# Kernel optimization log

Measured on AMD Instinct MI355X. Metric: run time of the kernel, lower is better.

The kernel has to match this reference:

```python
import jax, jax.numpy as jnp
import numpy as np

T, B, D, H = 512, 64, 512, 512


def setup_inputs() -> dict:
    key = jax.random.key(0)
    k_x, k_wi, k_wh = jax.random.split(key, 3)
    x = jax.random.normal(k_x, (T, B, D), dtype=jnp.float32)
    h0 = jnp.zeros((B, H), dtype=jnp.float32)
    # orthogonal(sqrt(2))-like scale approximated with scaled normal weights
    Wi = jax.random.normal(k_wi, (D, 3 * H), dtype=jnp.float32) * (1.0 / np.sqrt(D))
    Wh = jax.random.normal(k_wh, (H, 3 * H), dtype=jnp.float32) * (1.0 / np.sqrt(H))
    bi = jnp.zeros((3 * H,), dtype=jnp.float32)
    bhn = jnp.zeros((H,), dtype=jnp.float32)
    return {"x": x, "h0": h0, "Wi": Wi, "Wh": Wh, "bi": bi, "bhn": bhn}


def reference(x, h0, Wi, Wh, bi, bhn):
    # Flax GRUCell scanned over time. Gate order: (r, z, n).
    # Input path has bias bi; hidden path is bias-free except candidate (bhn).
    def step(h, xt):
        gi = xt @ Wi + bi              # [B, 3H]
        gh = h @ Wh                    # [B, 3H]
        i_r, i_z, i_n = jnp.split(gi, 3, axis=-1)
        h_r, h_z, h_n = jnp.split(gh, 3, axis=-1)
        r = jax.nn.sigmoid(i_r + h_r)
        z = jax.nn.sigmoid(i_z + h_z)
        n = jnp.tanh(i_n + r * (h_n + bhn))
        h_new = (1.0 - z) * n + z * h  # [B, H]
        return h_new, h_new            # y == new hidden state in GRUCell

    _, ys = jax.lax.scan(step, h0, x)  # ys: [T, B, H]; final carry == ys[-1]
    return ys
```

## Files before the change

kernel.cpp:

```cpp
#include <hip/hip_runtime.h>


#define T_STEPS 512
#define NWORK 32
#define CWG 8
#define NCL 4
#define NB_LAUNCH 256
#define FSTRIDE 16

typedef __attribute__((ext_vector_type(8))) short bhalf8;
typedef __attribute__((ext_vector_type(4))) float floatx4;

__device__ inline float bf2f(unsigned short u) {
  union { unsigned u; float f; } v; v.u = ((unsigned)u) << 16; return v.f;
}
__device__ inline unsigned short f2bf(float f) {
  union { float f; unsigned u; } v; v.f = f;
  unsigned x = v.u;
  return (unsigned short)((x + 0x7fffu + ((x >> 16) & 1u)) >> 16);
}

__device__ inline void gload_lds16(const void* g, void* l) {
  __builtin_amdgcn_global_load_lds(
      (const __attribute__((address_space(1))) void*)g,
      (__attribute__((address_space(3))) void*)l, 16, 0, 0);
}

#define O_BAR 0
#define O_HB  4096
#define O_WIT 69632
#define O_WHT 1642496
#define O_GI  3215360
#define O_XB  103878656ULL
#define WS_NEED 137433088ULL

__device__ inline unsigned short* HS(char* ws, int t) {
  return (t == 0) ? (unsigned short*)(ws + O_HB)
                  : (unsigned short*)(ws + O_XB + (long)(t - 1) * 65536);
}

__global__ void prep_kernel(const float* __restrict__ x, const float* __restrict__ h0,
                            const float* __restrict__ Wi, const float* __restrict__ Wh,
                            char* __restrict__ ws) {
  unsigned short* Xb  = (unsigned short*)(ws + O_XB);
  unsigned short* WiT = (unsigned short*)(ws + O_WIT);
  unsigned short* WhT = (unsigned short*)(ws + O_WHT);
  unsigned short* Hb0 = (unsigned short*)(ws + O_HB);
  int* bar = (int*)(ws + O_BAR);
  const long NX = 16777216, NW = 786432, NH = 32768;
  const long total = NX + 2 * NW + NH + 1024;
  for (long i = (long)blockIdx.x * blockDim.x + threadIdx.x; i < total;
       i += (long)gridDim.x * blockDim.x) {
    if (i < NX) {
      Xb[i] = f2bf(x[i]);
    } else if (i < NX + NW) {
      long j = i - NX;
      long n = j >> 9, k = j & 511;
      WiT[j] = f2bf(Wi[k * 1536 + n]);
    } else if (i < NX + 2 * NW) {
      long j = i - NX - NW;
      long n = j >> 9, k = j & 511;
      WhT[j] = f2bf(Wh[k * 1536 + n]);
    } else if (i < NX + 2 * NW + NH) {
      long j = i - NX - 2 * NW;
      Hb0[j] = f2bf(h0[j]);
    } else {
      bar[i - (NX + 2 * NW + NH)] = 0;
    }
  }
}

__global__ void gi_gemm(const unsigned short* __restrict__ Xb,
                        const unsigned short* __restrict__ WiT,
                        const float* __restrict__ bi,
                        unsigned short* __restrict__ Gi) {
  __shared__ unsigned short As[128 * 32];
  __shared__ unsigned short Bs[128 * 32];
  const int tid  = threadIdx.x;
  const int m0   = blockIdx.x * 128;
  const int n0   = blockIdx.y * 128;
  const int lane = tid & 63, wv = tid >> 6;
  const int quad = lane >> 4, l16 = lane & 15;
  const int wm = (wv & 1) * 64, wn = (wv >> 1) * 64;
  const int sr = tid >> 1, sc = (tid & 1) * 16;

  floatx4 acc[4][4] = {};

  for (int kb = 0; kb < 16; ++kb) {
    const int k0 = kb * 32;
    __syncthreads();
    *(bhalf8*)(&As[sr * 32 + sc])     = *(const bhalf8*)(&Xb[(long)(m0 + sr) * 512 + k0 + sc]);
    *(bhalf8*)(&As[sr * 32 + sc + 8]) = *(const bhalf8*)(&Xb[(long)(m0 + sr) * 512 + k0 + sc + 8]);
    *(bhalf8*)(&Bs[sr * 32 + sc])     = *(const bhalf8*)(&WiT[(long)(n0 + sr) * 512 + k0 + sc]);
    *(bhalf8*)(&Bs[sr * 32 + sc + 8]) = *(const bhalf8*)(&WiT[(long)(n0 + sr) * 512 + k0 + sc + 8]);
    __syncthreads();

    bhalf8 af[4], bf[4];
#pragma unroll
    for (int i = 0; i < 4; ++i)
      af[i] = *(const bhalf8*)(&As[(wm + i * 16 + l16) * 32 + quad * 8]);
#pragma unroll
    for (int j = 0; j < 4; ++j)
      bf[j] = *(const bhalf8*)(&Bs[(wn + j * 16 + l16) * 32 + quad * 8]);
#pragma unroll
    for (int i = 0; i < 4; ++i)
#pragma unroll
      for (int j = 0; j < 4; ++j)
        acc[i][j] = __builtin_amdgcn_mfma_f32_16x16x32_bf16(af[i], bf[j], acc[i][j], 0, 0, 0);
  }

#pragma unroll
  for (int i = 0; i < 4; ++i)
#pragma unroll
    for (int j = 0; j < 4; ++j) {
      const int col = n0 + wn + j * 16 + l16;
      const float bv = bi[col];
#pragma unroll
      for (int r = 0; r < 4; ++r) {
        const int row = m0 + wm + i * 16 + quad * 4 + r;
        Gi[(long)row * 1536 + col] = f2bf(acc[i][j][r] + bv);
      }
    }
}

#define GRU_STEP(T_, CUR_, NXT_) do {                                              \
    const int t_ = (T_);                                                           \
    const unsigned short* hin  = HS(ws, t_);                                       \
    unsigned short*       hout = HS(ws, t_ + 1);                                   \
    bhalf8 af[16];                                                                 \
    if (fast) {                                                                    \
      const char* hbase = (const char*)hin + (size_t)cluster * 16384;              \
      _Pragma("unroll")                                                            \
      for (int it = 0; it < 4; ++it) {                                             \
        const int row = wv * 4 + it;                       \
        const char* src = hbase + row * 1024 + ((lane * 16) ^ ((row & 15) << 5));  \
        gload_lds16(src, &smem[row * 1024]);        \
      }                                                                            \
      __syncthreads();         \
      _Pragma("unroll")                                                            \
      for (int ks = 0; ks < 16; ++ks) {                                            \
        const int byteoff =                                                        \
            (l16 << 10) + (((ks << 6) + (quad << 4)) ^ ((l16 & 15) << 5));         \
        af[ks] = *(const bhalf8*)(&smem[byteoff]);                                 \
      }                                                                            \
    } else {                                                                       \
      const unsigned short* ap = hin + (cluster * 16 + l16) * 512 + quad * 8;      \
      _Pragma("unroll")                                                            \
      for (int ks = 0; ks < 16; ++ks) {                                            \
        union { unsigned long long q[2]; bhalf8 v; } u;                            \
        u.q[0] = __hip_atomic_load((const unsigned long long*)(ap + ks * 32),      \
                                   __ATOMIC_RELAXED, __HIP_MEMORY_SCOPE_AGENT);    \
        u.q[1] = __hip_atomic_load((const unsigned long long*)(ap + ks * 32) + 1,  \
                                   __ATOMIC_RELAXED, __HIP_MEMORY_SCOPE_AGENT);    \
        af[ks] = u.v;                                                              \
      }                                                                            \
    }                                                                              \
    floatx4 racc = {0.f, 0.f, 0.f, 0.f};                                           \
    floatx4 zacc = {0.f, 0.f, 0.f, 0.f};                                           \
    floatx4 nacc = {0.f, 0.f, 0.f, 0.f};                                           \
    _Pragma("unroll")                                                              \
    for (int ks = 0; ks < 16; ++ks) {                                              \
      racc = __builtin_amdgcn_mfma_f32_16x16x32_bf16(af[ks], Bf[0][ks], racc, 0, 0, 0);\
      zacc = __builtin_amdgcn_mfma_f32_16x16x32_bf16(af[ks], Bf[1][ks], zacc, 0, 0, 0);\
      nacc = __builtin_amdgcn_mfma_f32_16x16x32_bf16(af[ks], Bf[2][ks], nacc, 0, 0, 0);\
    }                                                                              \
    _Pragma("unroll")                                                              \
    for (int r = 0; r < 4; ++r) {                                                  \
      const float rg = 1.f / (1.f + __expf(-(bf2f(CUR_[r]) + racc[r])));           \
      const float zg = 1.f / (1.f + __expf(-(bf2f(CUR_[4 + r]) + zacc[r])));       \
      const float pre = bf2f(CUR_[8 + r]) + rg * (nacc[r] + bhn_v);                \
      const float e2 = __expf(2.f * pre);                                          \
      const float ng = 1.f - 2.f / (e2 + 1.f);                           \
      const float hn = (1.f - zg) * ng + zg * hprev[r];                            \
      hprev[r] = hn;                                                               \
      const unsigned hb = (unsigned)f2bf(hn);                                      \
      const unsigned ob = __shfl_xor(hb, 1, 64);          \
      if (!(l16 & 1)) {                                                            \
        unsigned* dst = (unsigned*)(hout + (brow0 + r) * 512 + gcol);              \
        const unsigned packed = hb | (ob << 16);                                   \
        if (fast) *dst = packed;                      \
        else __hip_atomic_store(dst, packed, __ATOMIC_RELAXED,                     \
                                __HIP_MEMORY_SCOPE_AGENT);                         \
      }                                                                            \
    }                                                                              \
    if (t_ + 1 < T_STEPS) {                                                        \
      const int want = t_ + 1;                                                     \
      if (fast) {                                                                  \
        __syncthreads();                         \
        if (tid == 0)                                                              \
          __hip_atomic_store(&fflag[(cluster * CWG + slot) * FSTRIDE], want,       \
                             __ATOMIC_RELAXED, __HIP_MEMORY_SCOPE_AGENT);          \
                        \
        {                                                                          \
          bool ok = (lane >= CWG);                                                 \
          while (!__all(ok)) {                                                     \
            if (!ok) {                                                             \
              const int v = __hip_atomic_load(                                     \
                  &fflag[(cluster * CWG + lane) * FSTRIDE],                        \
                  __ATOMIC_RELAXED, __HIP_MEMORY_SCOPE_AGENT);                     \
              ok = (v >= want);                                                    \
            }                                                                      \
          }                                                                        \
        }                                                                          \
         \
        _Pragma("unroll")                                                          \
        for (int r = 0; r < 4; ++r)                                                \
          out[((long)t_ * 64 + brow0 + r) * 512 + gcol] = hprev[r];                \
        {                                                                          \
          const long gibase = (long)want * 64 * 1536;                              \
          _Pragma("unroll")                                                        \
          for (int r = 0; r < 4; ++r) {                                            \
            const long gb = gibase + (long)(brow0 + r) * 1536 + gcol;              \
            NXT_[r]     = Gi[gb];               \
            NXT_[4 + r] = Gi[gb + 512];          \
            NXT_[8 + r] = Gi[gb + 1024];                                           \
          }                                                                        \
        }                                                                          \
      } else {                                                                     \
        _Pragma("unroll")                                                          \
        for (int r = 0; r < 4; ++r)                                                \
          out[((long)t_ * 64 + brow0 + r) * 512 + gcol] = hprev[r];                \
        {                                                                          \
          const long gibase = (long)want * 64 * 1536;                              \
          _Pragma("unroll")                                                        \
          for (int r = 0; r < 4; ++r) {                                            \
            const long gb = gibase + (long)(brow0 + r) * 1536 + gcol;              \
            NXT_[r]     = Gi[gb];                                                  \
            NXT_[4 + r] = Gi[gb + 512];                                            \
            NXT_[8 + r] = Gi[gb + 1024];                                           \
          }                                                                        \
        }                                                                          \
        __syncthreads();                                                           \
        if (tid == 0)                                                              \
          __hip_atomic_store(&flags[cluster * CWG + slot], want,                   \
                             __ATOMIC_RELAXED, __HIP_MEMORY_SCOPE_AGENT);          \
        int v;                                                                     \
        do {                                                                       \
          v = __hip_atomic_load(&flags[cluster * CWG + (lane & 7)],                \
                                __ATOMIC_RELAXED, __HIP_MEMORY_SCOPE_AGENT);       \
        } while (!__all(v >= want));                                               \
        __atomic_signal_fence(__ATOMIC_SEQ_CST);                                   \
      }                                                                            \
    } else {                                                                       \
      _Pragma("unroll")                                                            \
      for (int r = 0; r < 4; ++r)                                                  \
        out[((long)t_ * 64 + brow0 + r) * 512 + gcol] = hprev[r];                  \
    }                                                                              \
  } while (0)

__launch_bounds__(256, 1)
__global__ void recurrent_kernel(char* __restrict__ ws,
                                 const float* __restrict__ h0,
                                 const float* __restrict__ bhn,
                                 float* __restrict__ out) {
  const unsigned short* WhT = (const unsigned short*)(ws + O_WHT);
  const unsigned short* Gi  = (const unsigned short*)(ws + O_GI);
  int* bar     = (int*)(ws + O_BAR);
  int* fflag   = bar;
  int* flags   = bar + 512;
  int* tick    = bar + 544;
  int* arrived = bar + 552;
  int* tick2   = bar + 553;
  int* abortf  = bar + 555;
  int* arrive2 = bar + 556;

  const int tid = threadIdx.x;
  __shared__ __align__(64) unsigned char smem[16384];
  __shared__ int sdec[4];

  if (tid == 0) {
    const int xcc = (int)(__builtin_amdgcn_s_getreg((3 << 11) | 20)) & 7;
    const int slot = __hip_atomic_fetch_add(&tick[xcc], 1, __ATOMIC_SEQ_CST, __HIP_MEMORY_SCOPE_AGENT);
    __hip_atomic_fetch_add(arrived, 1, __ATOMIC_SEQ_CST, __HIP_MEMORY_SCOPE_AGENT);
    while (__hip_atomic_load(arrived, __ATOMIC_ACQUIRE, __HIP_MEMORY_SCOPE_AGENT) < NB_LAUNCH)
      __builtin_amdgcn_s_sleep(4);
    int cnts[8];
    for (int c = 0; c < 8; ++c)
      cnts[c] = __hip_atomic_load(&tick[c], __ATOMIC_ACQUIRE, __HIP_MEMORY_SCOPE_AGENT);
    int chosen[NCL]; bool used[8] = {false,false,false,false,false,false,false,false};
    for (int k = 0; k < NCL; ++k) {
      int best = -1, bi2 = 0;
      for (int c = 0; c < 8; ++c)
        if (!used[c] && cnts[c] > best) { best = cnts[c]; bi2 = c; }
      chosen[k] = bi2; used[bi2] = true;
    }
    const int fastc = (cnts[chosen[NCL - 1]] >= CWG) ? 1 : 0;
    int cl = -1, sl = -1;
    if (fastc) {
      for (int k = 0; k < NCL; ++k)
        if (xcc == chosen[k] && slot < CWG) { cl = k; sl = slot; }
    } else {
      const int s2 = __hip_atomic_fetch_add(tick2, 1, __ATOMIC_SEQ_CST, __HIP_MEMORY_SCOPE_AGENT);
      if (s2 < NWORK) { cl = s2 >> 3; sl = s2 & 7; }
    }
    sdec[0] = fastc; sdec[1] = cl; sdec[2] = sl;
  }
  __syncthreads();
  const int fastc   = sdec[0];
  const int cluster = sdec[1];
  const int slot    = sdec[2];
  if (cluster < 0) return;

  if (tid == 0) {
    int mode = 0;
    if (fastc) {
      int* pc = bar + 576 + cluster * 16;
      __hip_atomic_fetch_add(pc, 1, __ATOMIC_RELAXED, __HIP_MEMORY_SCOPE_WORKGROUP);
      int ok = 0;
      for (int it = 0; it < 200000; ++it) {
        int exp = CWG;
        if (__hip_atomic_compare_exchange_strong(pc, &exp, CWG,
                __ATOMIC_RELAXED, __ATOMIC_RELAXED, __HIP_MEMORY_SCOPE_WORKGROUP)) { ok = 1; break; }
      }
      if (!ok) __hip_atomic_fetch_add(abortf, 1, __ATOMIC_RELAXED, __HIP_MEMORY_SCOPE_AGENT);
      __hip_atomic_fetch_add(arrive2, 1, __ATOMIC_ACQ_REL, __HIP_MEMORY_SCOPE_AGENT);
      while (__hip_atomic_load(arrive2, __ATOMIC_ACQUIRE, __HIP_MEMORY_SCOPE_AGENT) < NWORK)
        __builtin_amdgcn_s_sleep(2);
      mode = (__hip_atomic_load(abortf, __ATOMIC_ACQUIRE, __HIP_MEMORY_SCOPE_AGENT) > 0) ? 0 : 1;
    }
    sdec[3] = mode;
  }
  __syncthreads();
  const int fast = sdec[3];

  const int wv   = tid >> 6;
  const int lane = tid & 63;
  const int quad = lane >> 4, l16 = lane & 15;
  const int gcol = slot * 64 + wv * 16 + l16;
  const int brow0 = cluster * 16 + quad * 4;

  bhalf8 Bf[3][16];
#pragma unroll
  for (int gt = 0; gt < 3; ++gt) {
    const unsigned short* wp = WhT + (long)(gt * 512 + gcol) * 512;
#pragma unroll
    for (int ks = 0; ks < 16; ++ks)
      Bf[gt][ks] = *(const bhalf8*)(wp + ks * 32 + quad * 8);
  }
  const float bhn_v = bhn[gcol];

  float hprev[4];
#pragma unroll
  for (int r = 0; r < 4; ++r)
    hprev[r] = h0[(brow0 + r) * 512 + gcol];

  unsigned short giA[12], giB[12];
#pragma unroll
  for (int r = 0; r < 4; ++r) {
    const long gb = (long)(brow0 + r) * 1536 + gcol;
    giA[r]     = Gi[gb];
    giA[4 + r] = Gi[gb + 512];
    giA[8 + r] = Gi[gb + 1024];
  }

#pragma unroll 1
  for (int tt = 0; tt < T_STEPS; tt += 2) {
    GRU_STEP(tt,     giA, giB);
    GRU_STEP(tt + 1, giB, giA);
  }
}

extern "C" void kernel_launch(void* const* d_in, const int* in_sizes, int n_in,
                              void* d_out, int out_size, void* d_ws, size_t ws_size,
                              hipStream_t stream) {
  const float* x   = (const float*)d_in[0];
  const float* h0  = (const float*)d_in[1];
  const float* Wi  = (const float*)d_in[2];
  const float* Wh  = (const float*)d_in[3];
  const float* bi  = (const float*)d_in[4];
  const float* bhn = (const float*)d_in[5];
  float* out = (float*)d_out;
  char* ws = (char*)d_ws;
  if (ws_size < WS_NEED) return;

  prep_kernel<<<4096, 256, 0, stream>>>(x, h0, Wi, Wh, ws);
  gi_gemm<<<dim3(256, 12), 256, 0, stream>>>(
      (const unsigned short*)(ws + O_XB), (const unsigned short*)(ws + O_WIT),
      bi, (unsigned short*)(ws + O_GI));
  recurrent_kernel<<<NB_LAUNCH, 256, 0, stream>>>(ws, h0, bhn, out);
}
```

Before: 1.589 ms.

## Replace per-workgroup barrier flags with per-wave flags and prefetch Gi two steps ahead

In the fast path, the per-step __syncthreads and single workgroup flag are replaced. Each wave now publishes its own flag after draining its stores with s_waitcnt, and every wave polls all 32 wave flags of its cluster. The output write and the Gi load for step t+2 are moved before the spin-wait so they overlap with waiting on other waves. Gi is now double-buffered two steps ahead, and the flag stride is reduced. The cost is more flag traffic per poll, and a wave may race ahead of its siblings into LDS reuse without a barrier, which could be a correctness risk.

```diff
diff --git a/kernel.cpp b/kernel.cpp
--- a/kernel.cpp
+++ b/kernel.cpp
@@ -6,7 +6,7 @@
 #define CWG 8
 #define NCL 4
 #define NB_LAUNCH 256
-#define FSTRIDE 16
+#define FSTRIDE 4
 
 typedef __attribute__((ext_vector_type(8))) short bhalf8;
 typedef __attribute__((ext_vector_type(4))) float floatx4;
@@ -123,7 +123,7 @@
     }
 }
 
-#define GRU_STEP(T_, CUR_, NXT_) do {                                              \
+#define GRU_STEP(T_, CUR_) do {                                                    \
     const int t_ = (T_);                                                           \
     const unsigned short* hin  = HS(ws, t_);                                       \
     unsigned short*       hout = HS(ws, t_ + 1);                                   \
@@ -136,7 +136,7 @@
         const char* src = hbase + row * 1024 + ((lane * 16) ^ ((row & 15) << 5));  \
         gload_lds16(src, &smem[row * 1024]);        \
       }                                                                            \
-      __syncthreads();         \
+      __syncthreads();      \
       _Pragma("unroll")                                                            \
       for (int ks = 0; ks < 16; ++ks) {                                            \
         const int byteoff =                                                        \
@@ -186,48 +186,49 @@
     if (t_ + 1 < T_STEPS) {                                                        \
       const int want = t_ + 1;                                                     \
       if (fast) {                                                                  \
-        __syncthreads();                         \
-        if (tid == 0)                                                              \
-          __hip_atomic_store(&fflag[(cluster * CWG + slot) * FSTRIDE], want,       \
+                 \
+        asm volatile("s_waitcnt vmcnt(0)" ::: "memory");                           \
+        if (lane == 0)                                                             \
+          __hip_atomic_store(&fflag[(cluster * 32 + wslot) * FSTRIDE], want,       \
                              __ATOMIC_RELAXED, __HIP_MEMORY_SCOPE_AGENT);          \
-                        \
+                \
+        _Pragma("unroll")                                                          \
+        for (int r = 0; r < 4; ++r)                                                \
+          out[((long)t_ * 64 + brow0 + r) * 512 + gcol] = hprev[r];                \
+        if (t_ + 2 < T_STEPS) {                                                    \
+          const long gibase = (long)(t_ + 2) * 64 * 1536;                          \
+          _Pragma("unroll")                                                        \
+          for (int r = 0; r < 4; ++r) {                                            \
+            const long gb = gibase + (long)(brow0 + r) * 1536 + gcol;              \
+            CUR_[r]     = Gi[gb];                  \
+            CUR_[4 + r] = Gi[gb + 512];                                            \
+            CUR_[8 + r] = Gi[gb + 1024];                                           \
+          }                                                                        \
+        }                                                                          \
+                      \
         {                                                                          \
-          bool ok = (lane >= CWG);                                                 \
+          bool ok = (lane >= 32);                                                  \
           while (!__all(ok)) {                                                     \
             if (!ok) {                                                             \
               const int v = __hip_atomic_load(                                     \
-                  &fflag[(cluster * CWG + lane) * FSTRIDE],                        \
+                  &fflag[(cluster * 32 + lane) * FSTRIDE],                         \
                   __ATOMIC_RELAXED, __HIP_MEMORY_SCOPE_AGENT);                     \
               ok = (v >= want);                                                    \
             }                                                                      \
-          }                                                                        \
-        }                                                                          \
-         \
-        _Pragma("unroll")                                                          \
-        for (int r = 0; r < 4; ++r)                                                \
-          out[((long)t_ * 64 + brow0 + r) * 512 + gcol] = hprev[r];                \
-        {                                                                          \
-          const long gibase = (long)want * 64 * 1536;                              \
-          _Pragma("unroll")                                                        \
-          for (int r = 0; r < 4; ++r) {                                            \
-            const long gb = gibase + (long)(brow0 + r) * 1536 + gcol;              \
-            NXT_[r]     = Gi[gb];               \
-            NXT_[4 + r] = Gi[gb + 512];          \
-            NXT_[8 + r] = Gi[gb + 1024];                                           \
           }                                                                        \
         }                                                                          \
       } else {                                                                     \
         _Pragma("unroll")                                                          \
         for (int r = 0; r < 4; ++r)                                                \
           out[((long)t_ * 64 + brow0 + r) * 512 + gcol] = hprev[r];                \
-        {                                                                          \
-          const long gibase = (long)want * 64 * 1536;                              \
+        if (t_ + 2 < T_STEPS) {                                                    \
+          const long gibase = (long)(t_ + 2) * 64 * 1536;                          \
           _Pragma("unroll")                                                        \
           for (int r = 0; r < 4; ++r) {                                            \
             const long gb = gibase + (long)(brow0 + r) * 1536 + gcol;              \
-            NXT_[r]     = Gi[gb];                                                  \
-            NXT_[4 + r] = Gi[gb + 512];                                            \
-            NXT_[8 + r] = Gi[gb + 1024];                                           \
+            CUR_[r]     = Gi[gb];                                                  \
+            CUR_[4 + r] = Gi[gb + 512];                                            \
+            CUR_[8 + r] = Gi[gb + 1024];                                           \
           }                                                                        \
         }                                                                          \
         __syncthreads();                                                           \
@@ -322,12 +323,14 @@
   }
   __syncthreads();
   const int fast = sdec[3];
+  __syncthreads();
 
   const int wv   = tid >> 6;
   const int lane = tid & 63;
   const int quad = lane >> 4, l16 = lane & 15;
   const int gcol = slot * 64 + wv * 16 + l16;
   const int brow0 = cluster * 16 + quad * 4;
+  const int wslot = slot * 4 + wv;
 
   bhalf8 Bf[3][16];
 #pragma unroll
@@ -351,12 +354,16 @@
     giA[r]     = Gi[gb];
     giA[4 + r] = Gi[gb + 512];
     giA[8 + r] = Gi[gb + 1024];
+    const long gb1 = gb + 64 * 1536;
+    giB[r]     = Gi[gb1];
+    giB[4 + r] = Gi[gb1 + 512];
+    giB[8 + r] = Gi[gb1 + 1024];
   }
 
 #pragma unroll 1
   for (int tt = 0; tt < T_STEPS; tt += 2) {
-    GRU_STEP(tt,     giA, giB);
-    GRU_STEP(tt + 1, giB, giA);
+    GRU_STEP(tt,     giA);
+    GRU_STEP(tt + 1, giB);
   }
 }
 
```

New measurement: 1.548 ms. 1.03x faster.
